# Kernel tuning notes

Measured on AMD Instinct MI355X. Metric: run time of the kernel, lower is better.

Reference implementation:

```python
import jax, jax.numpy as jnp
import numpy as np

N_NODES = 50000
N_EDGES = 300000
F_IN = 11
D = 256


def _gcn_conv(h, src, dst, deg_inv_sqrt, W, b, n):
    """PyG GCNConv: out = D^{-1/2} (A + I) D^{-1/2} (h W) + b.
    src/dst already include self-loops; deg_inv_sqrt precomputed."""
    norm = deg_inv_sqrt[src] * deg_inv_sqrt[dst]          # [E+N]
    hw = h @ W                                            # [N, D]
    msg = hw[src] * norm[:, None]                         # [E+N, D]
    out = jax.ops.segment_sum(msg, dst, num_segments=n)   # [N, D]
    return out + b


def setup_inputs() -> dict:
    key = jax.random.key(0)
    ks = jax.random.split(key, 8)
    x = jax.random.normal(ks[0], (N_NODES, F_IN), dtype=jnp.float32)
    edge_index = jax.random.randint(ks[1], (2, N_EDGES), 0, N_NODES, dtype=jnp.int32)
    s = 0.05
    W_embed = jax.random.normal(ks[2], (F_IN, D), dtype=jnp.float32) * s
    b_embed = jnp.zeros((D,), dtype=jnp.float32)
    W1 = jax.random.normal(ks[3], (D, D), dtype=jnp.float32) * s
    b1 = jnp.zeros((D,), dtype=jnp.float32)
    W2 = jax.random.normal(ks[4], (D, D), dtype=jnp.float32) * s
    b2 = jnp.zeros((D,), dtype=jnp.float32)
    return {"x": x, "edge_index": edge_index, "W_embed": W_embed, "b_embed": b_embed,
            "W1": W1, "b1": b1, "W2": W2, "b2": b2}


def reference(x, edge_index, W_embed, b_embed, W1, b1, W2, b2):
    n = x.shape[0]
    # add self-loops (PyG GCNConv default add_self_loops=True)
    loop = jnp.arange(n, dtype=edge_index.dtype)
    src = jnp.concatenate([edge_index[0], loop])
    dst = jnp.concatenate([edge_index[1], loop])
    # symmetric normalization: deg over target index with unit edge weights
    deg = jax.ops.segment_sum(jnp.ones(src.shape, dtype=x.dtype), dst, num_segments=n)
    deg_inv_sqrt = jnp.where(deg > 0, jax.lax.rsqrt(jnp.maximum(deg, 1e-12)), 0.0)

    h = jax.nn.relu(x @ W_embed + b_embed)                # embed + relu
    h = jax.nn.relu(_gcn_conv(h, src, dst, deg_inv_sqrt, W1, b1, n))
    h = _gcn_conv(h, src, dst, deg_inv_sqrt, W2, b2, n)
    return h
```

## Files before the change

### kernel.cpp

```cpp
#include <hip/hip_runtime.h>

#define N_NODES 50000
#define N_EDGES 300000
#define N_TOT   350000
#define D       256
#define MPAD    50048
#define SCAN_B  196

typedef __attribute__((ext_vector_type(8))) short bf16x8;
typedef __attribute__((ext_vector_type(4))) float f32x4;
typedef __attribute__((ext_vector_type(8))) unsigned short u16x8;

__device__ __forceinline__ float bf2f(unsigned short b) {
    union { unsigned u; float f; } v; v.u = ((unsigned)b) << 16; return v.f;
}
__device__ __forceinline__ unsigned short f2bf(float f) {
    union { float f; unsigned u; } v; v.f = f;
    unsigned u = v.u;
    unsigned r = (u + 0x7FFFu + ((u >> 16) & 1u)) >> 16;
    return (unsigned short)r;
}
__device__ __forceinline__ void g2lds16(const unsigned short* g, unsigned short* l) {
    __builtin_amdgcn_global_load_lds(
        (const __attribute__((address_space(1))) void*)g,
        (__attribute__((address_space(3))) void*)l, 16, 0, 0);
}

__global__ __launch_bounds__(256) void prep1_kernel(
        const float* __restrict__ x, const float* __restrict__ We,
        const float* __restrict__ be, const float* __restrict__ W1,
        const float* __restrict__ W2,
        int* __restrict__ cnt, int* __restrict__ fc,
        unsigned short* __restrict__ Wt1, unsigned short* __restrict__ Wt2,
        unsigned short* __restrict__ hA) {
    int t = threadIdx.x;
    int tid = blockIdx.x * 256 + t;
    const int T = 512 * 256;
    for (int i = tid; i < N_NODES; i += T) { cnt[i] = 0; fc[i] = 0; }
    for (int i = tid; i < 2 * D * D; i += T) {
        int wsel = i >> 16, rem = i & 65535;
        int tt = rem >> 8, b = rem & 255;
        const float* W = wsel ? W2 : W1;
        unsigned short* Wt = wsel ? Wt2 : Wt1;
        Wt[b * D + tt] = f2bf(W[tt * D + b]);
    }
    float w[11];
    #pragma unroll
    for (int k = 0; k < 11; ++k) w[k] = We[k * D + t];
    float bb = be[t];
    for (int g = blockIdx.x; g < MPAD / 8; g += 512) {
        #pragma unroll
        for (int ni = 0; ni < 8; ++ni) {
            int node = g * 8 + ni;
            float acc = 0.f;
            if (node < N_NODES) {
                acc = bb;
                #pragma unroll
                for (int k = 0; k < 11; ++k) acc += x[node * 11 + k] * w[k];
                acc = fmaxf(acc, 0.f);
            }
            hA[(size_t)node * D + t] = f2bf(acc);
        }
    }
}

__global__ void hist_kernel(const int* __restrict__ ei, int* __restrict__ cnt) {
    int e = blockIdx.x * 256 + threadIdx.x;
    if (e >= N_TOT) return;
    int dst = (e < N_EDGES) ? ei[N_EDGES + e] : (e - N_EDGES);
    atomicAdd(&cnt[dst], 1);
}

__global__ void prep2_kernel(const int* __restrict__ cnt, float* __restrict__ dis,
                             int* __restrict__ locs, int* __restrict__ bsum) {
    __shared__ int ws[4];
    int t = threadIdx.x, lane = t & 63, wv = t >> 6;
    int i = blockIdx.x * 256 + t;
    int v = (i < N_NODES) ? cnt[i] : 0;
    if (i < N_NODES) dis[i] = rsqrtf((float)v);
    int s = v;
    #pragma unroll
    for (int d = 1; d < 64; d <<= 1) {
        int u = __shfl_up(s, d, 64);
        if (lane >= d) s += u;
    }
    if (lane == 63) ws[wv] = s;
    __syncthreads();
    int off = 0;
    #pragma unroll
    for (int k = 0; k < 4; ++k) if (k < wv) off += ws[k];
    s += off;
    if (i < N_NODES) locs[i] = s;
    if (t == 255) bsum[blockIdx.x] = s;
}

__global__ void scan2_kernel(int* __restrict__ bsum) {
    __shared__ int ws[4];
    int t = threadIdx.x, lane = t & 63, wv = t >> 6;
    int v = (t < SCAN_B) ? bsum[t] : 0;
    int s = v;
    #pragma unroll
    for (int d = 1; d < 64; d <<= 1) {
        int u = __shfl_up(s, d, 64);
        if (lane >= d) s += u;
    }
    if (lane == 63) ws[wv] = s;
    __syncthreads();
    int off = 0;
    #pragma unroll
    for (int k = 0; k < 4; ++k) if (k < wv) off += ws[k];
    s += off;
    if (t < SCAN_B) bsum[t] = s - v;
}

__global__ void prep3_kernel(const int* __restrict__ ei, const int* __restrict__ locs,
                             const int* __restrict__ bsum, const float* __restrict__ dis,
                             int* __restrict__ fc, int* __restrict__ rowptr,
                             int* __restrict__ esrc, float* __restrict__ enorm) {
    int tid = blockIdx.x * 256 + threadIdx.x;
    if (tid == 0) rowptr[0] = 0;
    if (tid < N_NODES)
        rowptr[tid + 1] = locs[tid] + bsum[tid >> 8];
    if (tid < N_TOT) {
        int src, dst;
        if (tid < N_EDGES) { src = ei[tid]; dst = ei[N_EDGES + tid]; }
        else               { src = dst = tid - N_EDGES; }
        int base = bsum[dst >> 8] + ((dst & 255) ? locs[dst - 1] : 0);
        int pos = base + atomicAdd(&fc[dst], 1);
        esrc[pos]  = src;
        enorm[pos] = dis[src] * dis[dst];
    }
}

__global__ __launch_bounds__(256) void gemm_kernel(const unsigned short* __restrict__ A,
                                                   const unsigned short* __restrict__ Bt,
                                                   unsigned short* __restrict__ C) {
    __shared__ unsigned short lA[128 * 32];
    __shared__ unsigned short lB[128 * 32];
    int t = threadIdx.x;
    int wv = t >> 6, lane = t & 63;
    int m0 = blockIdx.x * 128;
    int n0 = blockIdx.y * 128;
    int moff = (wv & 1) * 64, noff = (wv >> 1) * 64;
    int q = lane >> 4, r = lane & 15;

    int srow = t >> 2;
    int skof = (t & 3) * 8;

    const unsigned short* Ag0 = A  + (size_t)(m0 + srow) * D + skof;
    const unsigned short* Ag1 = Ag0 + (size_t)64 * D;
    const unsigned short* Bg0 = Bt + (size_t)(n0 + srow) * D + skof;
    const unsigned short* Bg1 = Bg0 + (size_t)64 * D;
    unsigned short* lA0 = lA + t * 8;
    unsigned short* lA1 = lA0 + 64 * 32;
    unsigned short* lB0 = lB + t * 8;
    unsigned short* lB1 = lB0 + 64 * 32;

    f32x4 acc[4][4] = {};
    for (int kk = 0; kk < D; kk += 32) {
        __syncthreads();
        g2lds16(Ag0 + kk, lA0);
        g2lds16(Ag1 + kk, lA1);
        g2lds16(Bg0 + kk, lB0);
        g2lds16(Bg1 + kk, lB1);
        __syncthreads();
        bf16x8 a[4], b[4];
        #pragma unroll
        for (int mt = 0; mt < 4; ++mt)
            a[mt] = *(const bf16x8*)(lA + (moff + mt * 16 + r) * 32 + q * 8);
        #pragma unroll
        for (int nt = 0; nt < 4; ++nt)
            b[nt] = *(const bf16x8*)(lB + (noff + nt * 16 + r) * 32 + q * 8);
        #pragma unroll
        for (int mt = 0; mt < 4; ++mt)
            #pragma unroll
            for (int nt = 0; nt < 4; ++nt)
                acc[mt][nt] = __builtin_amdgcn_mfma_f32_16x16x32_bf16(a[mt], b[nt], acc[mt][nt], 0, 0, 0);
    }
    #pragma unroll
    for (int mt = 0; mt < 4; ++mt)
        #pragma unroll
        for (int nt = 0; nt < 4; ++nt) {
            int col  = n0 + noff + nt * 16 + r;
            int rowb = m0 + moff + mt * 16 + q * 4;
            #pragma unroll
            for (int i = 0; i < 4; ++i)
                C[(size_t)(rowb + i) * D + col] = f2bf(acc[mt][nt][i]);
        }
}

__global__ __launch_bounds__(256) void agg_kernel(const unsigned short* __restrict__ hw,
                                                  const int* __restrict__ rowptr,
                                                  const int* __restrict__ esrc,
                                                  const float* __restrict__ enorm,
                                                  const float* __restrict__ bias,
                                                  unsigned short* __restrict__ out_bf,
                                                  float* __restrict__ out_f32,
                                                  int mode) {
    int wid  = threadIdx.x >> 6;
    int lane = threadIdx.x & 63;
    int node = blockIdx.x * 4 + wid;
    if (node >= N_NODES) return;
    int s0 = rowptr[node], s1 = rowptr[node + 1];
    int half = lane >> 5, hl = lane & 31;

    float acc[8] = {};
    for (int base = s0; base < s1; base += 64) {
        int ec = s1 - base; if (ec > 64) ec = 64;
        int   srcl = 0; float nml = 0.f;
        if (lane < ec) { srcl = esrc[base + lane]; nml = enorm[base + lane]; }
        int it = (ec + 1) >> 1;
        for (int i = 0; i < it; ++i) {
            int   e  = 2 * i + half;
            int   s  = __shfl(srcl, e, 64);
            float nm = __shfl(nml, e, 64);
            u16x8 hv = *(const u16x8*)(hw + (size_t)s * D + hl * 8);
            #pragma unroll
            for (int k = 0; k < 8; ++k) acc[k] += nm * bf2f(hv[k]);
        }
    }
    #pragma unroll
    for (int k = 0; k < 8; ++k) acc[k] += __shfl_xor(acc[k], 32, 64);

    if (lane < 32) {
        int c = hl * 8;
        float4 bv0 = *(const float4*)(bias + c);
        float4 bv1 = *(const float4*)(bias + c + 4);
        acc[0] += bv0.x; acc[1] += bv0.y; acc[2] += bv0.z; acc[3] += bv0.w;
        acc[4] += bv1.x; acc[5] += bv1.y; acc[6] += bv1.z; acc[7] += bv1.w;
        if (mode) {
            u16x8 ov;
            #pragma unroll
            for (int k = 0; k < 8; ++k) ov[k] = f2bf(fmaxf(acc[k], 0.f));
            *(u16x8*)(out_bf + (size_t)node * D + c) = ov;
        } else {
            float4 o0 = { acc[0], acc[1], acc[2], acc[3] };
            float4 o1 = { acc[4], acc[5], acc[6], acc[7] };
            *(float4*)(out_f32 + (size_t)node * D + c)     = o0;
            *(float4*)(out_f32 + (size_t)node * D + c + 4) = o1;
        }
    }
}

extern "C" void kernel_launch(void* const* d_in, const int* in_sizes, int n_in,
                              void* d_out, int out_size, void* d_ws, size_t ws_size,
                              hipStream_t stream) {
    const float* x  = (const float*)d_in[0];
    const int*   ei = (const int*)d_in[1];
    const float* We = (const float*)d_in[2];
    const float* be = (const float*)d_in[3];
    const float* W1 = (const float*)d_in[4];
    const float* b1 = (const float*)d_in[5];
    const float* W2 = (const float*)d_in[6];
    const float* b2 = (const float*)d_in[7];
    float* out = (float*)d_out;

    char* w = (char*)d_ws;
    auto alloc = [&](size_t bytes) {
        char* p = w;
        w += (bytes + 255) & ~(size_t)255;
        return p;
    };
    int*            cnt    = (int*)alloc((size_t)N_NODES * 4);
    int*            fc     = (int*)alloc((size_t)N_NODES * 4);
    int*            rowptr = (int*)alloc((size_t)(N_NODES + 1) * 4);
    int*            locs   = (int*)alloc((size_t)N_NODES * 4);
    int*            bsum   = (int*)alloc((size_t)SCAN_B * 4);
    float*          dis    = (float*)alloc((size_t)N_NODES * 4);
    int*            esrc   = (int*)alloc((size_t)N_TOT * 4);
    float*          enorm  = (float*)alloc((size_t)N_TOT * 4);
    unsigned short* Wt1    = (unsigned short*)alloc((size_t)D * D * 2);
    unsigned short* Wt2    = (unsigned short*)alloc((size_t)D * D * 2);
    unsigned short* hA     = (unsigned short*)alloc((size_t)MPAD * D * 2);
    unsigned short* hW     = (unsigned short*)alloc((size_t)MPAD * D * 2);

    prep1_kernel<<<512, 256, 0, stream>>>(x, We, be, W1, W2, cnt, fc, Wt1, Wt2, hA);
    hist_kernel<<<(N_TOT + 255) / 256, 256, 0, stream>>>(ei, cnt);
    prep2_kernel<<<SCAN_B, 256, 0, stream>>>(cnt, dis, locs, bsum);
    scan2_kernel<<<1, 256, 0, stream>>>(bsum);
    prep3_kernel<<<(N_TOT + 255) / 256, 256, 0, stream>>>(ei, locs, bsum, dis, fc,
                                                          rowptr, esrc, enorm);

    dim3 ggrid(MPAD / 128, 2);
    gemm_kernel<<<ggrid, 256, 0, stream>>>(hA, Wt1, hW);
    agg_kernel<<<(N_NODES + 3) / 4, 256, 0, stream>>>(hW, rowptr, esrc, enorm, b1, hA, nullptr, 1);

    gemm_kernel<<<ggrid, 256, 0, stream>>>(hA, Wt2, hW);
    agg_kernel<<<(N_NODES + 3) / 4, 256, 0, stream>>>(hW, rowptr, esrc, enorm, b2, nullptr, out, 0);
}
```

Before: 255.5 us.

## Fuse preprocessing kernels, drop edge-norm array, column-slice the aggregation

Merges histogram, weight transpose and embedding into one kernel, folds the block-sum scan into the prefix kernel with a last-block-done atomic, and zeroes counters with a memset. This cuts the number of launches. The per-edge norm array is removed: aggregation now gathers dis[src] and scales by dis[dst] at the end. Aggregation is restructured so each block covers a 32-column slice of 16 nodes, with 4 edges in flight per wave and 4-byte gathers. The narrower gathers may lower memory efficiency, and the extra dis lookup adds indirection.

```diff
diff --git a/kernel.cpp b/kernel.cpp
--- a/kernel.cpp
+++ b/kernel.cpp
@@ -26,54 +26,52 @@
         (__attribute__((address_space(3))) void*)l, 16, 0, 0);
 }
 
-__global__ __launch_bounds__(256) void prep1_kernel(
-        const float* __restrict__ x, const float* __restrict__ We,
-        const float* __restrict__ be, const float* __restrict__ W1,
-        const float* __restrict__ W2,
-        int* __restrict__ cnt, int* __restrict__ fc,
+__global__ __launch_bounds__(256) void k1_kernel(
+        const float* __restrict__ x, const int* __restrict__ ei,
+        const float* __restrict__ We, const float* __restrict__ be,
+        const float* __restrict__ W1, const float* __restrict__ W2,
+        int* __restrict__ cnt,
         unsigned short* __restrict__ Wt1, unsigned short* __restrict__ Wt2,
         unsigned short* __restrict__ hA) {
-    int t = threadIdx.x;
-    int tid = blockIdx.x * 256 + t;
-    const int T = 512 * 256;
-    for (int i = tid; i < N_NODES; i += T) { cnt[i] = 0; fc[i] = 0; }
-    for (int i = tid; i < 2 * D * D; i += T) {
-        int wsel = i >> 16, rem = i & 65535;
-        int tt = rem >> 8, b = rem & 255;
+    int t = threadIdx.x, b = blockIdx.x;
+    int tid = b * 256 + t;
+
+    if (tid < N_TOT) {
+        int dst = (tid < N_EDGES) ? ei[N_EDGES + tid] : (tid - N_EDGES);
+        atomicAdd(&cnt[dst], 1);
+    }
+    if (tid < 2 * D * D) {
+        int wsel = tid >> 16, rem = tid & 65535;
+        int tt = rem >> 8, bb = rem & 255;
         const float* W = wsel ? W2 : W1;
         unsigned short* Wt = wsel ? Wt2 : Wt1;
-        Wt[b * D + tt] = f2bf(W[tt * D + b]);
+        Wt[bb * D + tt] = f2bf(W[tt * D + bb]);
     }
     float w[11];
     #pragma unroll
     for (int k = 0; k < 11; ++k) w[k] = We[k * D + t];
     float bb = be[t];
-    for (int g = blockIdx.x; g < MPAD / 8; g += 512) {
-        #pragma unroll
-        for (int ni = 0; ni < 8; ++ni) {
-            int node = g * 8 + ni;
-            float acc = 0.f;
-            if (node < N_NODES) {
-                acc = bb;
-                #pragma unroll
-                for (int k = 0; k < 11; ++k) acc += x[node * 11 + k] * w[k];
-                acc = fmaxf(acc, 0.f);
-            }
-            hA[(size_t)node * D + t] = f2bf(acc);
-        }
-    }
-}
-
-__global__ void hist_kernel(const int* __restrict__ ei, int* __restrict__ cnt) {
-    int e = blockIdx.x * 256 + threadIdx.x;
-    if (e >= N_TOT) return;
-    int dst = (e < N_EDGES) ? ei[N_EDGES + e] : (e - N_EDGES);
-    atomicAdd(&cnt[dst], 1);
-}
-
-__global__ void prep2_kernel(const int* __restrict__ cnt, float* __restrict__ dis,
-                             int* __restrict__ locs, int* __restrict__ bsum) {
+    #pragma unroll
+    for (int ni = 0; ni < 8; ++ni) {
+        int node = b * 8 + ni;
+        float acc = 0.f;
+        if (node < N_NODES) {
+            acc = bb;
+            #pragma unroll
+            for (int k = 0; k < 11; ++k) acc += x[node * 11 + k] * w[k];
+            acc = fmaxf(acc, 0.f);
+        }
+        hA[(size_t)node * D + t] = f2bf(acc);
+    }
+}
+
+__global__ __launch_bounds__(256) void k2_kernel(const int* __restrict__ cnt,
+                                                 float* __restrict__ dis,
+                                                 int* __restrict__ locs,
+                                                 int* __restrict__ bsum,
+                                                 int* __restrict__ done) {
     __shared__ int ws[4];
+    __shared__ int amLast;
     int t = threadIdx.x, lane = t & 63, wv = t >> 6;
     int i = blockIdx.x * 256 + t;
     int v = (i < N_NODES) ? cnt[i] : 0;
@@ -91,32 +89,38 @@
     for (int k = 0; k < 4; ++k) if (k < wv) off += ws[k];
     s += off;
     if (i < N_NODES) locs[i] = s;
-    if (t == 255) bsum[blockIdx.x] = s;
-}
-
-__global__ void scan2_kernel(int* __restrict__ bsum) {
-    __shared__ int ws[4];
-    int t = threadIdx.x, lane = t & 63, wv = t >> 6;
-    int v = (t < SCAN_B) ? bsum[t] : 0;
-    int s = v;
-    #pragma unroll
-    for (int d = 1; d < 64; d <<= 1) {
-        int u = __shfl_up(s, d, 64);
-        if (lane >= d) s += u;
-    }
-    if (lane == 63) ws[wv] = s;
+
+    if (t == 255) {
+        bsum[blockIdx.x] = s;
+        __threadfence();
+        amLast = (atomicAdd(done, 1) == SCAN_B - 1);
+    }
     __syncthreads();
-    int off = 0;
-    #pragma unroll
-    for (int k = 0; k < 4; ++k) if (k < wv) off += ws[k];
-    s += off;
-    if (t < SCAN_B) bsum[t] = s - v;
-}
-
-__global__ void prep3_kernel(const int* __restrict__ ei, const int* __restrict__ locs,
-                             const int* __restrict__ bsum, const float* __restrict__ dis,
-                             int* __restrict__ fc, int* __restrict__ rowptr,
-                             int* __restrict__ esrc, float* __restrict__ enorm) {
+    if (amLast) {
+        __threadfence();
+        int vv = 0;
+        if (t < SCAN_B)
+            vv = __hip_atomic_load(&bsum[t], __ATOMIC_RELAXED, __HIP_MEMORY_SCOPE_AGENT);
+        int ss = vv;
+        #pragma unroll
+        for (int d = 1; d < 64; d <<= 1) {
+            int u = __shfl_up(ss, d, 64);
+            if (lane >= d) ss += u;
+        }
+        __syncthreads();
+        if (lane == 63) ws[wv] = ss;
+        __syncthreads();
+        int off2 = 0;
+        #pragma unroll
+        for (int k = 0; k < 4; ++k) if (k < wv) off2 += ws[k];
+        ss += off2;
+        if (t < SCAN_B) bsum[t] = ss - vv;
+    }
+}
+
+__global__ void k3_kernel(const int* __restrict__ ei, const int* __restrict__ locs,
+                          const int* __restrict__ bsum, int* __restrict__ fc,
+                          int* __restrict__ rowptr, int* __restrict__ esrc) {
     int tid = blockIdx.x * 256 + threadIdx.x;
     if (tid == 0) rowptr[0] = 0;
     if (tid < N_NODES)
@@ -127,8 +131,7 @@
         else               { src = dst = tid - N_EDGES; }
         int base = bsum[dst >> 8] + ((dst & 255) ? locs[dst - 1] : 0);
         int pos = base + atomicAdd(&fc[dst], 1);
-        esrc[pos]  = src;
-        enorm[pos] = dis[src] * dis[dst];
+        esrc[pos] = src;
     }
 }
 
@@ -192,52 +195,53 @@
 __global__ __launch_bounds__(256) void agg_kernel(const unsigned short* __restrict__ hw,
                                                   const int* __restrict__ rowptr,
                                                   const int* __restrict__ esrc,
-                                                  const float* __restrict__ enorm,
+                                                  const float* __restrict__ dis,
                                                   const float* __restrict__ bias,
                                                   unsigned short* __restrict__ out_bf,
                                                   float* __restrict__ out_f32,
                                                   int mode) {
-    int wid  = threadIdx.x >> 6;
-    int lane = threadIdx.x & 63;
-    int node = blockIdx.x * 4 + wid;
-    if (node >= N_NODES) return;
-    int s0 = rowptr[node], s1 = rowptr[node + 1];
-    int half = lane >> 5, hl = lane & 31;
-
-    float acc[8] = {};
-    for (int base = s0; base < s1; base += 64) {
-        int ec = s1 - base; if (ec > 64) ec = 64;
-        int   srcl = 0; float nml = 0.f;
-        if (lane < ec) { srcl = esrc[base + lane]; nml = enorm[base + lane]; }
-        int it = (ec + 1) >> 1;
-        for (int i = 0; i < it; ++i) {
-            int   e  = 2 * i + half;
-            int   s  = __shfl(srcl, e, 64);
-            float nm = __shfl(nml, e, 64);
-            u16x8 hv = *(const u16x8*)(hw + (size_t)s * D + hl * 8);
-            #pragma unroll
-            for (int k = 0; k < 8; ++k) acc[k] += nm * bf2f(hv[k]);
-        }
-    }
-    #pragma unroll
-    for (int k = 0; k < 8; ++k) acc[k] += __shfl_xor(acc[k], 32, 64);
-
-    if (lane < 32) {
-        int c = hl * 8;
-        float4 bv0 = *(const float4*)(bias + c);
-        float4 bv1 = *(const float4*)(bias + c + 4);
-        acc[0] += bv0.x; acc[1] += bv0.y; acc[2] += bv0.z; acc[3] += bv0.w;
-        acc[4] += bv1.x; acc[5] += bv1.y; acc[6] += bv1.z; acc[7] += bv1.w;
-        if (mode) {
-            u16x8 ov;
-            #pragma unroll
-            for (int k = 0; k < 8; ++k) ov[k] = f2bf(fmaxf(acc[k], 0.f));
-            *(u16x8*)(out_bf + (size_t)node * D + c) = ov;
-        } else {
-            float4 o0 = { acc[0], acc[1], acc[2], acc[3] };
-            float4 o1 = { acc[4], acc[5], acc[6], acc[7] };
-            *(float4*)(out_f32 + (size_t)node * D + c)     = o0;
-            *(float4*)(out_f32 + (size_t)node * D + c + 4) = o1;
+    int b = blockIdx.x;
+    int slice = b & 7;
+    int chunk = b >> 3;
+    int wv = threadIdx.x >> 6, lane = threadIdx.x & 63;
+    int sub = lane >> 4, cl = lane & 15;
+    int colbase = slice * 32 + cl * 2;
+
+    #pragma unroll
+    for (int ni = 0; ni < 4; ++ni) {
+        int node = chunk * 16 + wv * 4 + ni;
+        if (node >= N_NODES) break;
+        int s0 = rowptr[node], s1 = rowptr[node + 1];
+        float a0 = 0.f, a1 = 0.f;
+        for (int base = s0; base < s1; base += 64) {
+            int ec = s1 - base; if (ec > 64) ec = 64;
+            int srcl = 0; float dsl = 0.f;
+            if (lane < ec) { srcl = esrc[base + lane]; dsl = dis[srcl]; }
+            int it = (ec + 3) >> 2;
+            for (int i = 0; i < it; ++i) {
+                int   e  = 4 * i + sub;
+                int   s  = __shfl(srcl, e, 64);
+                float dv = __shfl(dsl, e, 64);
+                unsigned hv = *(const unsigned*)(hw + (size_t)s * D + colbase);
+                a0 += dv * bf2f((unsigned short)(hv & 0xffffu));
+                a1 += dv * bf2f((unsigned short)(hv >> 16));
+            }
+        }
+        a0 += __shfl_xor(a0, 16, 64); a0 += __shfl_xor(a0, 32, 64);
+        a1 += __shfl_xor(a1, 16, 64); a1 += __shfl_xor(a1, 32, 64);
+        if (lane < 16) {
+            float dn = dis[node];
+            float2 bv = *(const float2*)(bias + colbase);
+            float v0 = dn * a0 + bv.x;
+            float v1 = dn * a1 + bv.y;
+            if (mode) {
+                v0 = fmaxf(v0, 0.f); v1 = fmaxf(v1, 0.f);
+                unsigned pv = (unsigned)f2bf(v0) | ((unsigned)f2bf(v1) << 16);
+                *(unsigned*)(out_bf + (size_t)node * D + colbase) = pv;
+            } else {
+                float2 o = { v0, v1 };
+                *(float2*)(out_f32 + (size_t)node * D + colbase) = o;
+            }
         }
     }
 }
@@ -263,28 +267,28 @@
     };
     int*            cnt    = (int*)alloc((size_t)N_NODES * 4);
     int*            fc     = (int*)alloc((size_t)N_NODES * 4);
+    int*            done   = (int*)alloc(4);
+    size_t zero_span = (size_t)((char*)(done + 64) - (char*)cnt);
     int*            rowptr = (int*)alloc((size_t)(N_NODES + 1) * 4);
     int*            locs   = (int*)alloc((size_t)N_NODES * 4);
     int*            bsum   = (int*)alloc((size_t)SCAN_B * 4);
     float*          dis    = (float*)alloc((size_t)N_NODES * 4);
     int*            esrc   = (int*)alloc((size_t)N_TOT * 4);
-    float*          enorm  = (float*)alloc((size_t)N_TOT * 4);
     unsigned short* Wt1    = (unsigned short*)alloc((size_t)D * D * 2);
     unsigned short* Wt2    = (unsigned short*)alloc((size_t)D * D * 2);
     unsigned short* hA     = (unsigned short*)alloc((size_t)MPAD * D * 2);
     unsigned short* hW     = (unsigned short*)alloc((size_t)MPAD * D * 2);
 
-    prep1_kernel<<<512, 256, 0, stream>>>(x, We, be, W1, W2, cnt, fc, Wt1, Wt2, hA);
-    hist_kernel<<<(N_TOT + 255) / 256, 256, 0, stream>>>(ei, cnt);
-    prep2_kernel<<<SCAN_B, 256, 0, stream>>>(cnt, dis, locs, bsum);
-    scan2_kernel<<<1, 256, 0, stream>>>(bsum);
-    prep3_kernel<<<(N_TOT + 255) / 256, 256, 0, stream>>>(ei, locs, bsum, dis, fc,
-                                                          rowptr, esrc, enorm);
+    hipMemsetAsync(cnt, 0, zero_span, stream);
+    k1_kernel<<<MPAD / 8, 256, 0, stream>>>(x, ei, We, be, W1, W2, cnt, Wt1, Wt2, hA);
+    k2_kernel<<<SCAN_B, 256, 0, stream>>>(cnt, dis, locs, bsum, done);
+    k3_kernel<<<(N_TOT + 255) / 256, 256, 0, stream>>>(ei, locs, bsum, fc, rowptr, esrc);
 
     dim3 ggrid(MPAD / 128, 2);
+    const int AGG_GRID = ((N_NODES + 15) / 16) * 8;
     gemm_kernel<<<ggrid, 256, 0, stream>>>(hA, Wt1, hW);
-    agg_kernel<<<(N_NODES + 3) / 4, 256, 0, stream>>>(hW, rowptr, esrc, enorm, b1, hA, nullptr, 1);
+    agg_kernel<<<AGG_GRID, 256, 0, stream>>>(hW, rowptr, esrc, dis, b1, hA, nullptr, 1);
 
     gemm_kernel<<<ggrid, 256, 0, stream>>>(hA, Wt2, hW);
-    agg_kernel<<<(N_NODES + 3) / 4, 256, 0, stream>>>(hW, rowptr, esrc, enorm, b2, nullptr, out, 0);
-}
+    agg_kernel<<<AGG_GRID, 256, 0, stream>>>(hW, rowptr, esrc, dis, b2, nullptr, out, 0);
+}
```

Measured after the change: 373.2 us. 46.1% more time.
